# Optimization experiments

Hardware: AMD Instinct MI355X
Metric: run time of the kernel (lower is better)

## Reference

```python
import jax, jax.numpy as jnp
import numpy as np

N = 50000
E = 800000
NODE_IN, EDGE_IN, HID, OUT, L = 32, 16, 128, 128, 2


def _layer_norm(h, g, b, eps=1e-5):
    mu = jnp.mean(h, axis=-1, keepdims=True)
    var = jnp.var(h, axis=-1, keepdims=True)
    return (h - mu) * jax.lax.rsqrt(var + eps) * g + b


def setup_inputs() -> dict:
    key = jax.random.key(0)
    ks = jax.random.split(key, 20)
    s = lambda k, shape, fan: jax.random.normal(k, shape, jnp.float32) * (1.0 / np.sqrt(fan))
    return {
        "x": jax.random.normal(ks[0], (N, NODE_IN), jnp.float32),
        "edge_index": jax.random.randint(ks[1], (2, E), 0, N, jnp.int64),
        "edge_attr": jax.random.normal(ks[2], (E, EDGE_IN), jnp.float32),
        "enc_W": s(ks[3], (NODE_IN, HID), NODE_IN),
        "enc_b": jnp.zeros((HID,), jnp.float32),
        "enc_g": jnp.ones((HID,), jnp.float32),
        "enc_beta": jnp.zeros((HID,), jnp.float32),
        "msg_W1": s(ks[4], (L, 2 * HID + EDGE_IN, HID), 2 * HID + EDGE_IN),
        "msg_b1": jnp.zeros((L, HID), jnp.float32),
        "msg_W2": s(ks[5], (L, HID, HID), HID),
        "msg_b2": jnp.zeros((L, HID), jnp.float32),
        "upd_W1": s(ks[6], (L, 2 * HID, HID), 2 * HID),
        "upd_b1": jnp.zeros((L, HID), jnp.float32),
        "upd_W2": s(ks[7], (L, HID, HID), HID),
        "upd_b2": jnp.zeros((L, HID), jnp.float32),
        "ln_g": jnp.ones((L, HID), jnp.float32),
        "ln_beta": jnp.zeros((L, HID), jnp.float32),
        "head_W": s(ks[8], (HID, OUT), HID),
        "head_b": jnp.zeros((OUT,), jnp.float32),
    }


def reference(x, edge_index, edge_attr, enc_W, enc_b, enc_g, enc_beta,
              msg_W1, msg_b1, msg_W2, msg_b2, upd_W1, upd_b1, upd_W2, upd_b2,
              ln_g, ln_beta, head_W, head_b):
    src = edge_index[0]  # x_j (source)
    tgt = edge_index[1]  # x_i (target, aggregation index)
    n = x.shape[0]

    # node encoder: Linear -> ReLU -> LayerNorm
    h = jax.nn.relu(x @ enc_W + enc_b)
    h = _layer_norm(h, enc_g, enc_beta)

    # per-edge incoming-degree for mean aggregation (isolated nodes -> 0)
    cnt = jax.ops.segment_sum(jnp.ones((tgt.shape[0],), h.dtype), tgt, num_segments=n)
    denom = jnp.maximum(cnt, 1.0)[:, None]

    for l in range(L):
        x_i = h[tgt]                                 # [E, HID]
        x_j = h[src]                                 # [E, HID]
        msg_in = jnp.concatenate([x_i, x_j, edge_attr], axis=-1)  # [E, 2H+Ed]
        m = jax.nn.relu(msg_in @ msg_W1[l] + msg_b1[l]) @ msg_W2[l] + msg_b2[l]
        aggr = jax.ops.segment_sum(m, tgt, num_segments=n) / denom  # mean
        upd_in = jnp.concatenate([h, aggr], axis=-1)
        out = jax.nn.relu(upd_in @ upd_W1[l] + upd_b1[l]) @ upd_W2[l] + upd_b2[l]
        h = _layer_norm(h + out, ln_g[l], ln_beta[l])

    return h @ head_W + head_b
```

## Files before the change

### kernel.cpp

```cpp
#include <hip/hip_runtime.h>
#include <hip/hip_bf16.h>
#include <stdint.h>

#define N_NODES 50000
#define N_EDGES 800000
#define NL 2

#define KS2 136
#define KSU 264
#define ESTR 132

typedef __bf16 bf16x8 __attribute__((ext_vector_type(8)));
typedef float f32x4 __attribute__((ext_vector_type(4)));

__device__ __forceinline__ f32x4 mfma_bf16(uint4 a, uint4 b, f32x4 c) {
    return __builtin_amdgcn_mfma_f32_16x16x32_bf16(
        __builtin_bit_cast(bf16x8, a), __builtin_bit_cast(bf16x8, b), c, 0, 0, 0);
}

__device__ __forceinline__ unsigned short f2b(float f) {
    union { float f; unsigned u; } v; v.f = f;
    unsigned r = v.u + 0x7FFFu + ((v.u >> 16) & 1u);
    return (unsigned short)(r >> 16);
}

__device__ __forceinline__ float b2f(unsigned short u) {
    union { unsigned u; float f; } v; v.u = ((unsigned)u) << 16; return v.f;
}
__device__ __forceinline__ float b2f_lo(unsigned u) {
    union { unsigned u; float f; } v; v.u = u << 16; return v.f;
}
__device__ __forceinline__ float b2f_hi(unsigned u) {
    union { unsigned u; float f; } v; v.u = u & 0xFFFF0000u; return v.f;
}

template<int KSTEPS, int BSTR>
__device__ __forceinline__ void gemm8(const unsigned short* aLane,
                                      const unsigned short* bLane, f32x4 acc[8]) {
#pragma unroll
    for (int kc = 0; kc < KSTEPS; kc++) {
        uint4 a = *(const uint4*)(aLane + kc * 32);
#pragma unroll
        for (int ct = 0; ct < 8; ct++) {
            uint4 b = *(const uint4*)(bLane + (size_t)ct * 16 * BSTR + kc * 32);
            acc[ct] = mfma_bf16(a, b, acc[ct]);
        }
    }
}

template<int KSTEPS, int ASTR, int BSTR>
__device__ __forceinline__ void gemm_2x4(const unsigned short* aLane,
                                         const unsigned short* bLane,
                                         f32x4 acc[4][2]) {
#pragma unroll
    for (int kc = 0; kc < KSTEPS; kc++) {
        uint4 b0 = *(const uint4*)(bLane + kc * 32);
        uint4 b1 = *(const uint4*)(bLane + (size_t)16 * BSTR + kc * 32);
#pragma unroll
        for (int rt = 0; rt < 4; rt++) {
            uint4 a = *(const uint4*)(aLane + (size_t)rt * 16 * ASTR + kc * 32);
            acc[rt][0] = mfma_bf16(a, b0, acc[rt][0]);
            acc[rt][1] = mfma_bf16(a, b1, acc[rt][1]);
        }
    }
}

__global__ void prep_kernel(const float* __restrict__ mW1,
                            const float* __restrict__ uW1, const float* __restrict__ uW2,
                            const float* __restrict__ hW,
                            unsigned short* __restrict__ wab, unsigned short* __restrict__ w1cp,
                            unsigned short* __restrict__ u1t, unsigned short* __restrict__ u2t,
                            unsigned short* __restrict__ ht) {
    int i = blockIdx.x * 256 + threadIdx.x;
    const int SA = NL * 256 * 136;
    const int SC = NL * 128 * 32;
    const int SU = NL * 128 * KSU;
    const int S3 = NL * 128 * KS2;
    const int S4 = 128 * KS2;
    if (i < SA) {
        int l = i / (256 * 136), r = i % (256 * 136), j = r / 136, k = r % 136;
        float v = 0.f;
        if (k < 128)
            v = (j < 128) ? mW1[((size_t)l * 272 + k) * 128 + j]
                          : mW1[((size_t)l * 272 + 128 + k) * 128 + (j - 128)];
        wab[i] = f2b(v);
        return;
    }
    i -= SA;
    if (i < SC) {
        int l = i / (128 * 32), r = i % (128 * 32), j = r / 32, k = r % 32;
        w1cp[i] = (k < 16) ? f2b(mW1[((size_t)l * 272 + 256 + k) * 128 + j]) : (unsigned short)0;
        return;
    }
    i -= SC;
    if (i < SU) {
        int l = i / (128 * KSU), r = i % (128 * KSU), n = r / KSU, k = r % KSU;
        if (k < 128)       u1t[i] = f2b(uW1[((size_t)l * 256 + k) * 128 + n]);
        else if (k >= 256) u1t[i] = 0;
        return;
    }
    i -= SU;
    if (i < S3) {
        int l = i / (128 * KS2), r = i % (128 * KS2), n = r / KS2, k = r % KS2;
        u2t[i] = (k < 128) ? f2b(uW2[((size_t)l * 128 + k) * 128 + n]) : (unsigned short)0;
        return;
    }
    i -= S3;
    if (i < S4) {
        int n = i / KS2, k = i % KS2;
        ht[i] = (k < 128) ? f2b(hW[(size_t)k * 128 + n]) : (unsigned short)0;
    }
}

__global__ void prep2_kernel(const float* __restrict__ mW2, const float* __restrict__ uW1,
                             unsigned short* __restrict__ u1t) {
    __shared__ float w2row[128];
    const int l = blockIdx.x >> 7, j = blockIdx.x & 127;
    const int n = threadIdx.x;
    w2row[n] = mW2[((size_t)l * 128 + j) * 128 + n];
    __syncthreads();
    float s = 0.f;
#pragma unroll 8
    for (int c = 0; c < 128; c++)
        s += w2row[c] * uW1[((size_t)l * 256 + 128 + c) * 128 + n];
    u1t[(size_t)l * 128 * KSU + (size_t)n * KSU + 128 + j] = f2b(s);
}

__global__ void prep3_kernel(const float* __restrict__ mb2, const float* __restrict__ uW1,
                             float* __restrict__ bfold) {
    const int l = blockIdx.x;
    const int n = threadIdx.x;
    float s = 0.f;
#pragma unroll 8
    for (int c = 0; c < 128; c++)
        s += mb2[l * 128 + c] * uW1[((size_t)l * 256 + 128 + c) * 128 + n];
    bfold[l * 128 + n] = s;
}

__global__ __launch_bounds__(256) void enc_kernel(
        const float* __restrict__ x, const float* __restrict__ W,
        const float* __restrict__ b, const float* __restrict__ g, const float* __restrict__ bet,
        float* __restrict__ h, unsigned short* __restrict__ hb) {
    __shared__ float sx[64];
    __shared__ float redS[4], redSS[4];
    const int t = threadIdx.x;
    const int nb = blockIdx.x * 2;
    if (t < 64) sx[t] = x[(size_t)nb * 32 + t];
    __syncthreads();
    const int half = t >> 7, j = t & 127;
    const int node = nb + half;
    float acc = b[j];
#pragma unroll
    for (int k = 0; k < 32; k++) acc += sx[half * 32 + k] * W[k * 128 + j];
    float v = fmaxf(acc, 0.f);
    float s = v, ss = v * v;
#pragma unroll
    for (int d = 32; d > 0; d >>= 1) { s += __shfl_down(s, d); ss += __shfl_down(ss, d); }
    const int wv = t >> 6;
    if ((t & 63) == 0) { redS[wv] = s; redSS[wv] = ss; }
    __syncthreads();
    float S = redS[half * 2] + redS[half * 2 + 1];
    float SS = redSS[half * 2] + redSS[half * 2 + 1];
    float mu = S * (1.f / 128.f);
    float var = SS * (1.f / 128.f) - mu * mu;
    float rs = rsqrtf(var + 1e-5f);
    float o = (v - mu) * rs * g[j] + bet[j];
    h[(size_t)node * 128 + j] = o;
    hb[(size_t)node * 128 + j] = f2b(o);
}

__global__ void hist_kernel(const int* __restrict__ tgt, int* __restrict__ hist) {
    int i = blockIdx.x * 256 + threadIdx.x;
    atomicAdd(hist + tgt[i], 1);
}

__global__ void scan1_kernel(const int* __restrict__ hist, int* __restrict__ incl,
                             int* __restrict__ blksum) {
    __shared__ int buf[256];
    const int t = threadIdx.x;
    const int i = blockIdx.x * 256 + t;
    int v = (i < N_NODES) ? hist[i] : 0;
    buf[t] = v; __syncthreads();
#pragma unroll
    for (int d = 1; d < 256; d <<= 1) {
        int x = (t >= d) ? buf[t - d] : 0;
        __syncthreads();
        buf[t] += x;
        __syncthreads();
    }
    if (i < N_NODES) incl[i] = buf[t];
    if (t == 255) blksum[blockIdx.x] = buf[255];
}

__global__ void scan2_kernel(int* __restrict__ blksum, int nblk) {
    __shared__ int buf[256];
    const int t = threadIdx.x;
    int v = (t < nblk) ? blksum[t] : 0;
    buf[t] = v; __syncthreads();
#pragma unroll
    for (int d = 1; d < 256; d <<= 1) {
        int x = (t >= d) ? buf[t - d] : 0;
        __syncthreads();
        buf[t] += x;
        __syncthreads();
    }
    if (t < nblk) blksum[t] = buf[t];
}

__global__ void scan3_kernel(int* __restrict__ incl, const int* __restrict__ blksum,
                             const int* __restrict__ hist) {
    const int i = blockIdx.x * 256 + threadIdx.x;
    if (i >= N_NODES) return;
    const int b = blockIdx.x;
    const int base = (b > 0) ? blksum[b - 1] : 0;
    incl[i] = incl[i] + base - hist[i];
}

__global__ void scatterp_kernel(const int* __restrict__ src, const int* __restrict__ tgt,
                                int* __restrict__ cursor, uint2* __restrict__ permst) {
    const int e = blockIdx.x * 256 + threadIdx.x;
    const int tg = tgt[e];
    const int p = atomicAdd(cursor + tg, 1);
    permst[p] = make_uint2((unsigned)e, ((unsigned)src[e] << 16) | (unsigned)tg);
}

__global__ __launch_bounds__(256) void gather_kernel(
        const uint2* __restrict__ permst, const float* __restrict__ ea,
        unsigned int* __restrict__ sST, unsigned short* __restrict__ eabS) {
    const int p = blockIdx.x * 256 + threadIdx.x;
    const uint2 v = permst[p];
    sST[p] = v.y;
    const float4* s = (const float4*)(ea + (size_t)v.x * 16);
    ushort4* d = (ushort4*)(eabS + (size_t)p * 16);
#pragma unroll
    for (int i = 0; i < 4; i++) {
        float4 f = s[i];
        d[i] = make_ushort4(f2b(f.x), f2b(f.y), f2b(f.z), f2b(f.w));
    }
}

__global__ __launch_bounds__(256, 4) void node_kernel(
        const unsigned short* __restrict__ hb, const unsigned short* __restrict__ wab,
        const float* __restrict__ b1,
        unsigned short* __restrict__ Tb, unsigned short* __restrict__ Sb) {
    __shared__ __align__(16) unsigned short As[64 * KS2];
    const int t = threadIdx.x;
    const int n0 = blockIdx.x * 64;
    {
        const int m = t >> 2, q = t & 3;
        const int node = n0 + m;
        uint4* dst = (uint4*)(As + m * KS2);
        if (node < N_NODES) {
            const uint4* s = (const uint4*)(hb + (size_t)node * 128);
#pragma unroll
            for (int i = 0; i < 4; i++) dst[q * 4 + i] = s[q * 4 + i];
        } else {
            uint4 z{0, 0, 0, 0};
            for (int i = q; i < 16; i += 4) dst[i] = z;
        }
    }
    __syncthreads();

    const int wv = t >> 6, lane = t & 63, lr = lane & 15, lq = lane >> 4;
    const int cb = wv * 64;
    const f32x4 z4 = {0.f, 0.f, 0.f, 0.f};
    f32x4 acc[4][4];
#pragma unroll
    for (int i = 0; i < 4; i++)
#pragma unroll
        for (int j = 0; j < 4; j++) acc[i][j] = z4;

    const unsigned short* aL = As + lr * KS2 + lq * 8;
    const unsigned short* bL = wab + (size_t)(cb + lr) * KS2 + lq * 8;
#pragma unroll
    for (int kc = 0; kc < 4; kc++) {
        uint4 bA = *(const uint4*)(bL + kc * 32);
        uint4 bB = *(const uint4*)(bL + (size_t)16 * KS2 + kc * 32);
        uint4 bC = *(const uint4*)(bL + (size_t)32 * KS2 + kc * 32);
        uint4 bD = *(const uint4*)(bL + (size_t)48 * KS2 + kc * 32);
#pragma unroll
        for (int rt = 0; rt < 4; rt++) {
            uint4 a = *(const uint4*)(aL + (size_t)rt * 16 * KS2 + kc * 32);
            acc[rt][0] = mfma_bf16(a, bA, acc[rt][0]);
            acc[rt][1] = mfma_bf16(a, bB, acc[rt][1]);
            acc[rt][2] = mfma_bf16(a, bC, acc[rt][2]);
            acc[rt][3] = mfma_bf16(a, bD, acc[rt][3]);
        }
    }
#pragma unroll
    for (int ct = 0; ct < 4; ct++) {
        const int j = cb + ct * 16 + lr;
        const float bias = (j < 128) ? b1[j] : 0.f;
#pragma unroll
        for (int rt = 0; rt < 4; rt++) {
#pragma unroll
            for (int r = 0; r < 4; r++) {
                const int node = n0 + rt * 16 + lq * 4 + r;
                if (node < N_NODES) {
                    const float v = acc[rt][ct][r] + bias;
                    if (j < 128) Tb[(size_t)node * 128 + j] = f2b(v);
                    else         Sb[(size_t)node * 128 + (j - 128)] = f2b(v);
                }
            }
        }
    }
}

__global__ __launch_bounds__(256, 8) void edge_kernel(
        const unsigned short* __restrict__ eabS,
        const unsigned int* __restrict__ sST,
        const unsigned short* __restrict__ w1cp,
        const unsigned short* __restrict__ Tb, const unsigned short* __restrict__ Sb,
        float* __restrict__ aggr) {
    __shared__ __align__(16) float Es[32 * ESTR];
    __shared__ int sT[64];
    __shared__ int sS[64];

    const int t = threadIdx.x;
    const int e0 = blockIdx.x * 64;
    if (t < 64) {
        const unsigned v = sST[e0 + t];
        sT[t] = (int)(v & 0xFFFFu);
        sS[t] = (int)(v >> 16);
    }
    __syncthreads();

    const int wv = t >> 6, lane = t & 63, lr = lane & 15, lq = lane >> 4;
    const int rtw = (wv >> 1) * 16;
    const int cbw = (wv & 1) * 64;
    const int m = t & 31, c8b = t >> 5;
    const f32x4 z4 = {0.f, 0.f, 0.f, 0.f};

    unsigned long long bmask;
    {
        const int l = t & 63;
        const int a = sT[l];
        const int b = (l > 0) ? sT[l - 1] : a;
        bmask = __ballot(a != b);
    }

    uint4 t0a, t0b, s0a, s0b;
    {
        const unsigned short* Tr = Tb + (size_t)sT[m] * 128;
        const unsigned short* Sr = Sb + (size_t)sS[m] * 128;
        t0a = *(const uint4*)(Tr + c8b * 8);
        t0b = *(const uint4*)(Tr + c8b * 8 + 64);
        s0a = *(const uint4*)(Sr + c8b * 8);
        s0b = *(const uint4*)(Sr + c8b * 8 + 64);
    }

    float s = 0.f;
    bool first = true;

    {
        uint4 a = {0, 0, 0, 0};
        if (lq < 2)
            a = *(const uint4*)(eabS + (size_t)(e0 + rtw + lr) * 16 + lq * 8);
        f32x4 acc[4];
#pragma unroll
        for (int ct = 0; ct < 4; ct++) {
            uint4 b = *(const uint4*)(w1cp + (cbw + ct * 16 + lr) * 32 + lq * 8);
            acc[ct] = mfma_bf16(a, b, z4);
        }
#pragma unroll
        for (int ct = 0; ct < 4; ct++) {
            const int col = cbw + ct * 16 + lr;
#pragma unroll
            for (int r = 0; r < 4; r++)
                Es[(rtw + lq * 4 + r) * ESTR + col] = acc[ct][r];
        }
    }
    __syncthreads();

    uint4 t1a, t1b, s1a, s1b;
    {
        float* Erow = Es + m * ESTR;
        float4* EA = (float4*)(Erow + c8b * 8);
        float4* EB = (float4*)(Erow + c8b * 8 + 64);
        float4 ea0 = EA[0], ea1 = EA[1];
        ea0.x = fmaxf(ea0.x + b2f_lo(t0a.x) + b2f_lo(s0a.x), 0.f);
        ea0.y = fmaxf(ea0.y + b2f_hi(t0a.x) + b2f_hi(s0a.x), 0.f);
        ea0.z = fmaxf(ea0.z + b2f_lo(t0a.y) + b2f_lo(s0a.y), 0.f);
        ea0.w = fmaxf(ea0.w + b2f_hi(t0a.y) + b2f_hi(s0a.y), 0.f);
        ea1.x = fmaxf(ea1.x + b2f_lo(t0a.z) + b2f_lo(s0a.z), 0.f);
        ea1.y = fmaxf(ea1.y + b2f_hi(t0a.z) + b2f_hi(s0a.z), 0.f);
        ea1.z = fmaxf(ea1.z + b2f_lo(t0a.w) + b2f_lo(s0a.w), 0.f);
        ea1.w = fmaxf(ea1.w + b2f_hi(t0a.w) + b2f_hi(s0a.w), 0.f);
        EA[0] = ea0; EA[1] = ea1;
        float4 eb0 = EB[0], eb1 = EB[1];
        eb0.x = fmaxf(eb0.x + b2f_lo(t0b.x) + b2f_lo(s0b.x), 0.f);
        eb0.y = fmaxf(eb0.y + b2f_hi(t0b.x) + b2f_hi(s0b.x), 0.f);
        eb0.z = fmaxf(eb0.z + b2f_lo(t0b.y) + b2f_lo(s0b.y), 0.f);
        eb0.w = fmaxf(eb0.w + b2f_hi(t0b.y) + b2f_hi(s0b.y), 0.f);
        eb1.x = fmaxf(eb1.x + b2f_lo(t0b.z) + b2f_lo(s0b.z), 0.f);
        eb1.y = fmaxf(eb1.y + b2f_hi(t0b.z) + b2f_hi(s0b.z), 0.f);
        eb1.z = fmaxf(eb1.z + b2f_lo(t0b.w) + b2f_lo(s0b.w), 0.f);
        eb1.w = fmaxf(eb1.w + b2f_hi(t0b.w) + b2f_hi(s0b.w), 0.f);
        EB[0] = eb0; EB[1] = eb1;

        const unsigned short* Tr = Tb + (size_t)sT[32 + m] * 128;
        const unsigned short* Sr = Sb + (size_t)sS[32 + m] * 128;
        t1a = *(const uint4*)(Tr + c8b * 8);
        t1b = *(const uint4*)(Tr + c8b * 8 + 64);
        s1a = *(const uint4*)(Sr + c8b * 8);
        s1b = *(const uint4*)(Sr + c8b * 8 + 64);
    }
    __syncthreads();

    if (t < 128) {
        const int c = t;
        const unsigned mh = (unsigned)bmask;
#pragma unroll
        for (int i8 = 0; i8 < 4; i8++) {
            float v[8];
#pragma unroll
            for (int j = 0; j < 8; j++) v[j] = Es[(i8 * 8 + j) * ESTR + c];
#pragma unroll
            for (int j = 0; j < 8; j++) {
                const int i = i8 * 8 + j;
                if (mh & (1u << i)) {
                    float* dst = aggr + (size_t)sT[i - 1] * 128 + c;
                    if (first) { atomicAdd(dst, s); first = false; }
                    else       { *dst = s; }
                    s = 0.f;
                }
                s += v[j];
            }
        }
    }
    __syncthreads();

    {
        uint4 a = {0, 0, 0, 0};
        if (lq < 2)
            a = *(const uint4*)(eabS + (size_t)(e0 + 32 + rtw + lr) * 16 + lq * 8);
        f32x4 acc[4];
#pragma unroll
        for (int ct = 0; ct < 4; ct++) {
            uint4 b = *(const uint4*)(w1cp + (cbw + ct * 16 + lr) * 32 + lq * 8);
            acc[ct] = mfma_bf16(a, b, z4);
        }
#pragma unroll
        for (int ct = 0; ct < 4; ct++) {
            const int col = cbw + ct * 16 + lr;
#pragma unroll
            for (int r = 0; r < 4; r++)
                Es[(rtw + lq * 4 + r) * ESTR + col] = acc[ct][r];
        }
    }
    __syncthreads();

    {
        float* Erow = Es + m * ESTR;
        float4* EA = (float4*)(Erow + c8b * 8);
        float4* EB = (float4*)(Erow + c8b * 8 + 64);
        float4 ea0 = EA[0], ea1 = EA[1];
        ea0.x = fmaxf(ea0.x + b2f_lo(t1a.x) + b2f_lo(s1a.x), 0.f);
        ea0.y = fmaxf(ea0.y + b2f_hi(t1a.x) + b2f_hi(s1a.x), 0.f);
        ea0.z = fmaxf(ea0.z + b2f_lo(t1a.y) + b2f_lo(s1a.y), 0.f);
        ea0.w = fmaxf(ea0.w + b2f_hi(t1a.y) + b2f_hi(s1a.y), 0.f);
        ea1.x = fmaxf(ea1.x + b2f_lo(t1a.z) + b2f_lo(s1a.z), 0.f);
        ea1.y = fmaxf(ea1.y + b2f_hi(t1a.z) + b2f_hi(s1a.z), 0.f);
        ea1.z = fmaxf(ea1.z + b2f_lo(t1a.w) + b2f_lo(s1a.w), 0.f);
        ea1.w = fmaxf(ea1.w + b2f_hi(t1a.w) + b2f_hi(s1a.w), 0.f);
        EA[0] = ea0; EA[1] = ea1;
        float4 eb0 = EB[0], eb1 = EB[1];
        eb0.x = fmaxf(eb0.x + b2f_lo(t1b.x) + b2f_lo(s1b.x), 0.f);
        eb0.y = fmaxf(eb0.y + b2f_hi(t1b.x) + b2f_hi(s1b.x), 0.f);
        eb0.z = fmaxf(eb0.z + b2f_lo(t1b.y) + b2f_lo(s1b.y), 0.f);
        eb0.w = fmaxf(eb0.w + b2f_hi(t1b.y) + b2f_hi(s1b.y), 0.f);
        eb1.x = fmaxf(eb1.x + b2f_lo(t1b.z) + b2f_lo(s1b.z), 0.f);
        eb1.y = fmaxf(eb1.y + b2f_hi(t1b.z) + b2f_hi(s1b.z), 0.f);
        eb1.z = fmaxf(eb1.z + b2f_lo(t1b.w) + b2f_lo(s1b.w), 0.f);
        eb1.w = fmaxf(eb1.w + b2f_hi(t1b.w) + b2f_hi(s1b.w), 0.f);
        EB[0] = eb0; EB[1] = eb1;
    }
    __syncthreads();

    if (t < 128) {
        const int c = t;
        const unsigned mh = (unsigned)(bmask >> 32);
#pragma unroll
        for (int i8 = 0; i8 < 4; i8++) {
            float v[8];
#pragma unroll
            for (int j = 0; j < 8; j++) v[j] = Es[(i8 * 8 + j) * ESTR + c];
#pragma unroll
            for (int j = 0; j < 8; j++) {
                const int i = i8 * 8 + j;
                if (mh & (1u << i)) {
                    float* dst = aggr + (size_t)sT[32 + i - 1] * 128 + c;
                    if (first) { atomicAdd(dst, s); first = false; }
                    else       { *dst = s; }
                    s = 0.f;
                }
                s += v[j];
            }
        }
        atomicAdd(aggr + (size_t)sT[63] * 128 + c, s);
    }
}

__global__ __launch_bounds__(256, 4) void upd_kernel(
        const unsigned short* __restrict__ hb_in, const float* __restrict__ h_in,
        const float* __restrict__ aggr, const int* __restrict__ hist,
        const unsigned short* __restrict__ u1t, const unsigned short* __restrict__ u2t,
        const float* __restrict__ b1, const float* __restrict__ bf,
        const float* __restrict__ b2,
        const float* __restrict__ g, const float* __restrict__ bet,
        float* __restrict__ h_out, unsigned short* __restrict__ hb_out) {
    __shared__ __align__(16) char smemA[64 * KSU * 2];
    __shared__ float sF[64];
    unsigned short* As = (unsigned short*)smemA;
    float* LNb = (float*)smemA;

    const int t = threadIdx.x;
    const int n0 = blockIdx.x * 64;
    {
        const int m = t >> 2, q = t & 3;
        const int node = n0 + m;
        unsigned short* row = As + m * KSU;
        if (node < N_NODES) {
            const uint4* ph = (const uint4*)(hb_in + (size_t)node * 128);
            uint4* d0 = (uint4*)row;
#pragma unroll
            for (int i = 0; i < 4; i++) d0[q * 4 + i] = ph[q * 4 + i];
            const int cntv = hist[node];
            if (q == 0) sF[m] = (cntv > 0) ? 1.f : 0.f;
            const float rden = 1.0f / fmaxf((float)cntv, 1.0f);
            const float4* pa = (const float4*)(aggr + (size_t)node * 128 + q * 32);
            ushort4* d1 = (ushort4*)(row + 128 + q * 32);
#pragma unroll
            for (int i = 0; i < 8; i++) {
                float4 v = pa[i];
                d1[i] = make_ushort4(f2b(v.x * rden), f2b(v.y * rden),
                                     f2b(v.z * rden), f2b(v.w * rden));
            }
            if (q == 0) { uint4 z{0, 0, 0, 0}; ((uint4*)(row + 256))[0] = z; }
        } else {
            if (q == 0) sF[m] = 0.f;
            uint4 z{0, 0, 0, 0};
            uint4* d = (uint4*)row;
            for (int i = q; i < 33; i += 4) d[i] = z;
        }
    }
    __syncthreads();

    const int wv = t >> 6, lane = t & 63, lr = lane & 15, lq = lane >> 4;
    const int cb = wv * 32;
    const f32x4 z4 = {0.f, 0.f, 0.f, 0.f};

    f32x4 acc[4][2];
#pragma unroll
    for (int i = 0; i < 4; i++) { acc[i][0] = z4; acc[i][1] = z4; }
    gemm_2x4<8, KSU, KSU>(As + lr * KSU + lq * 8,
                          u1t + (size_t)(cb + lr) * KSU + lq * 8, acc);
    __syncthreads();

#pragma unroll
    for (int ct = 0; ct < 2; ct++) {
        const int col = cb + ct * 16 + lr;
        const float bv = b1[col];
        const float bfv = bf[col];
#pragma unroll
        for (int rt = 0; rt < 4; rt++) {
#pragma unroll
            for (int r = 0; r < 4; r++) {
                const int ml = rt * 16 + lq * 4 + r;
                float v = fmaxf(acc[rt][ct][r] + bv + sF[ml] * bfv, 0.f);
                As[ml * KSU + col] = f2b(v);
            }
        }
    }
    __syncthreads();

    f32x4 acc2[4][2];
#pragma unroll
    for (int i = 0; i < 4; i++) { acc2[i][0] = z4; acc2[i][1] = z4; }
    gemm_2x4<4, KSU, KS2>(As + lr * KSU + lq * 8,
                          u2t + (size_t)(cb + lr) * KS2 + lq * 8, acc2);
    __syncthreads();

#pragma unroll
    for (int ct = 0; ct < 2; ct++) {
        const int col = cb + ct * 16 + lr;
        const float bv = b2[col];
#pragma unroll
        for (int rt = 0; rt < 4; rt++) {
#pragma unroll
            for (int r = 0; r < 4; r++) {
                const int ml = rt * 16 + lq * 4 + r;
                const int node = n0 + ml;
                if (node < N_NODES)
                    LNb[ml * 132 + col] = acc2[rt][ct][r] + bv + h_in[(size_t)node * 128 + col];
            }
        }
    }
    __syncthreads();

    {
        const int r = t >> 2, c0 = (t & 3) * 32;
        const int node = n0 + r;
        if (node < N_NODES) {
            float s = 0.f, ss = 0.f;
#pragma unroll
            for (int i = 0; i < 32; i++) { float v = LNb[r * 132 + c0 + i]; s += v; ss += v * v; }
            s += __shfl_xor(s, 1); ss += __shfl_xor(ss, 1);
            s += __shfl_xor(s, 2); ss += __shfl_xor(ss, 2);
            const float mu = s * (1.0f / 128.0f);
            const float var = ss * (1.0f / 128.0f) - mu * mu;
            const float rs = rsqrtf(var + 1e-5f);
#pragma unroll
            for (int i = 0; i < 32; i++) {
                const int j = c0 + i;
                float v = (LNb[r * 132 + j] - mu) * rs * g[j] + bet[j];
                h_out[(size_t)node * 128 + j] = v;
                hb_out[(size_t)node * 128 + j] = f2b(v);
            }
        }
    }
}

__global__ __launch_bounds__(256, 2) void head_kernel(
        const unsigned short* __restrict__ hb, const unsigned short* __restrict__ ht,
        const float* __restrict__ hbias, float* __restrict__ out) {
    __shared__ __align__(16) unsigned short As[64 * KS2];
    const int t = threadIdx.x;
    const int n0 = blockIdx.x * 64;
    {
        const int m = t >> 2, q = t & 3;
        const int node = n0 + m;
        uint4* dst = (uint4*)(As + m * KS2);
        if (node < N_NODES) {
            const uint4* s = (const uint4*)(hb + (size_t)node * 128);
#pragma unroll
            for (int i = 0; i < 4; i++) dst[q * 4 + i] = s[q * 4 + i];
        } else {
            uint4 z{0, 0, 0, 0};
            for (int i = q; i < 16; i += 4) dst[i] = z;
        }
    }
    __syncthreads();

    const int wv = t >> 6, lane = t & 63, lr = lane & 15, lq = lane >> 4;
    const int m0 = wv * 16;
    const f32x4 z4 = {0.f, 0.f, 0.f, 0.f};
    f32x4 acc[8];
#pragma unroll
    for (int i = 0; i < 8; i++) acc[i] = z4;
    gemm8<4, KS2>(As + (m0 + lr) * KS2 + lq * 8, ht + (size_t)lr * KS2 + lq * 8, acc);
#pragma unroll
    for (int ct = 0; ct < 8; ct++) {
        const int col = ct * 16 + lr;
        const float bv = hbias[col];
#pragma unroll
        for (int r = 0; r < 4; r++) {
            const int node = n0 + m0 + lq * 4 + r;
            if (node < N_NODES) out[(size_t)node * 128 + col] = acc[ct][r] + bv;
        }
    }
}

extern "C" void kernel_launch(void* const* d_in, const int* in_sizes, int n_in,
                              void* d_out, int out_size, void* d_ws, size_t ws_size,
                              hipStream_t stream) {
    const float* x       = (const float*)d_in[0];
    const int*   ei      = (const int*)d_in[1];
    const float* ea      = (const float*)d_in[2];
    const float* encW    = (const float*)d_in[3];
    const float* encb    = (const float*)d_in[4];
    const float* encg    = (const float*)d_in[5];
    const float* encbeta = (const float*)d_in[6];
    const float* msgW1   = (const float*)d_in[7];
    const float* msgb1   = (const float*)d_in[8];
    const float* msgW2   = (const float*)d_in[9];
    const float* msgb2   = (const float*)d_in[10];
    const float* updW1   = (const float*)d_in[11];
    const float* updb1   = (const float*)d_in[12];
    const float* updW2   = (const float*)d_in[13];
    const float* updb2   = (const float*)d_in[14];
    const float* lng     = (const float*)d_in[15];
    const float* lnbeta  = (const float*)d_in[16];
    const float* headW   = (const float*)d_in[17];
    const float* headb   = (const float*)d_in[18];

    char* w = (char*)d_ws;
    size_t off = 0;
    auto nxt = [&](size_t bytes) -> void* {
        void* p = w + off;
        off = (off + bytes + 255) & ~(size_t)255;
        return p;
    };
    float*          h     = (float*)nxt((size_t)N_NODES * 128 * 4);
    unsigned short* hb    = (unsigned short*)nxt((size_t)N_NODES * 128 * 2);
    float*          aggr  = (float*)nxt((size_t)N_NODES * 128 * 4);
    unsigned short* Tb    = (unsigned short*)nxt((size_t)N_NODES * 128 * 2);
    unsigned short* Sb    = (unsigned short*)nxt((size_t)N_NODES * 128 * 2);
    unsigned short* eabS  = (unsigned short*)nxt((size_t)N_EDGES * 16 * 2);
    unsigned int*   sST   = (unsigned int*)nxt((size_t)N_EDGES * 4);
    int*            hist  = (int*)nxt((size_t)N_NODES * 4);
    int*            incl  = (int*)nxt((size_t)N_NODES * 4);
    int*            blksum= (int*)nxt(256 * 4);
    unsigned short* wab   = (unsigned short*)nxt((size_t)NL * 256 * 136 * 2);
    unsigned short* w1cp  = (unsigned short*)nxt((size_t)NL * 128 * 32 * 2);
    unsigned short* u1t   = (unsigned short*)nxt((size_t)NL * 128 * KSU * 2);
    unsigned short* u2t   = (unsigned short*)nxt((size_t)NL * 128 * KS2 * 2);
    unsigned short* ht    = (unsigned short*)nxt((size_t)128 * KS2 * 2);
    float*          bfold = (float*)nxt((size_t)NL * 128 * 4);

    uint2*          permst = (uint2*)aggr;

    const int NBLK = (N_NODES + 255) / 256;
    const int PREP_N = NL * 256 * 136 + NL * 128 * 32 + NL * 128 * KSU
                     + NL * 128 * KS2 + 128 * KS2;

    hipMemsetAsync(hist, 0, (size_t)N_NODES * 4, stream);
    prep_kernel<<<(PREP_N + 255) / 256, 256, 0, stream>>>(msgW1, updW1, updW2, headW,
                                                          wab, w1cp, u1t, u2t, ht);
    prep2_kernel<<<NL * 128, 128, 0, stream>>>(msgW2, updW1, u1t);
    prep3_kernel<<<NL, 128, 0, stream>>>(msgb2, updW1, bfold);
    enc_kernel<<<25000, 256, 0, stream>>>(x, encW, encb, encg, encbeta, h, hb);
    hist_kernel<<<3125, 256, 0, stream>>>(ei + N_EDGES, hist);
    scan1_kernel<<<NBLK, 256, 0, stream>>>(hist, incl, blksum);
    scan2_kernel<<<1, 256, 0, stream>>>(blksum, NBLK);
    scan3_kernel<<<NBLK, 256, 0, stream>>>(incl, blksum, hist);
    scatterp_kernel<<<3125, 256, 0, stream>>>(ei, ei + N_EDGES, incl, permst);
    gather_kernel<<<3125, 256, 0, stream>>>(permst, ea, sST, eabS);

    for (int l = 0; l < NL; l++) {
        node_kernel<<<782, 256, 0, stream>>>(hb, wab + (size_t)l * 256 * 136,
                                             msgb1 + l * 128, Tb, Sb);
        hipMemsetAsync(aggr, 0, (size_t)N_NODES * 128 * 4, stream);
        edge_kernel<<<12500, 256, 0, stream>>>(eabS, sST,
                                               w1cp + (size_t)l * 128 * 32,
                                               Tb, Sb, aggr);
        upd_kernel<<<782, 256, 0, stream>>>(hb, h, aggr, hist,
                                            u1t + (size_t)l * 128 * KSU,
                                            u2t + (size_t)l * 128 * KS2,
                                            updb1 + l * 128, bfold + l * 128,
                                            updb2 + l * 128,
                                            lng + l * 128, lnbeta + l * 128, h, hb);
    }
    head_kernel<<<782, 256, 0, stream>>>(hb, ht, headb, (float*)d_out);
}
```

Baseline: 550.5 us.

## Swizzle edge LDS tile and fuse head GEMM into final update kernel

In the edge kernel, the fp32 staging tile gets an XOR swizzle keyed on row, and gathered rows are remapped to 8 threads per edge, to cut LDS bank conflicts on both the MFMA-result stores and the row-wise vector reads. In the last layer, the update kernel now runs the output-head GEMM itself, reusing its shared memory for the bf16 normalized rows. This removes the separate head kernel launch and the final h/hb writes. The fused path adds two syncs and a 32-float register buffer per thread, which may raise register pressure in the update kernel.

```diff
diff --git a/kernel.cpp b/kernel.cpp
--- a/kernel.cpp
+++ b/kernel.cpp
@@ -328,7 +328,9 @@
     const int wv = t >> 6, lane = t & 63, lr = lane & 15, lq = lane >> 4;
     const int rtw = (wv >> 1) * 16;
     const int cbw = (wv & 1) * 64;
-    const int m = t & 31, c8b = t >> 5;
+    const int m = t >> 3;
+    const int q = t & 7;
+    const int sw = (m & 7) << 3;
     const f32x4 z4 = {0.f, 0.f, 0.f, 0.f};
 
     unsigned long long bmask;
@@ -343,10 +345,10 @@
     {
         const unsigned short* Tr = Tb + (size_t)sT[m] * 128;
         const unsigned short* Sr = Sb + (size_t)sS[m] * 128;
-        t0a = *(const uint4*)(Tr + c8b * 8);
-        t0b = *(const uint4*)(Tr + c8b * 8 + 64);
-        s0a = *(const uint4*)(Sr + c8b * 8);
-        s0b = *(const uint4*)(Sr + c8b * 8 + 64);
+        t0a = *(const uint4*)(Tr + q * 8);
+        t0b = *(const uint4*)(Tr + 64 + q * 8);
+        s0a = *(const uint4*)(Sr + q * 8);
+        s0b = *(const uint4*)(Sr + 64 + q * 8);
     }
 
     float s = 0.f;
@@ -366,8 +368,10 @@
         for (int ct = 0; ct < 4; ct++) {
             const int col = cbw + ct * 16 + lr;
 #pragma unroll
-            for (int r = 0; r < 4; r++)
-                Es[(rtw + lq * 4 + r) * ESTR + col] = acc[ct][r];
+            for (int r = 0; r < 4; r++) {
+                const int row = rtw + lq * 4 + r;
+                Es[row * ESTR + (col ^ ((row & 7) << 3))] = acc[ct][r];
+            }
         }
     }
     __syncthreads();
@@ -375,8 +379,8 @@
     uint4 t1a, t1b, s1a, s1b;
     {
         float* Erow = Es + m * ESTR;
-        float4* EA = (float4*)(Erow + c8b * 8);
-        float4* EB = (float4*)(Erow + c8b * 8 + 64);
+        float4* EA = (float4*)(Erow + ((q * 8) ^ sw));
+        float4* EB = (float4*)(Erow + 64 + ((q * 8) ^ sw));
         float4 ea0 = EA[0], ea1 = EA[1];
         ea0.x = fmaxf(ea0.x + b2f_lo(t0a.x) + b2f_lo(s0a.x), 0.f);
         ea0.y = fmaxf(ea0.y + b2f_hi(t0a.x) + b2f_hi(s0a.x), 0.f);
@@ -400,10 +404,10 @@
 
         const unsigned short* Tr = Tb + (size_t)sT[32 + m] * 128;
         const unsigned short* Sr = Sb + (size_t)sS[32 + m] * 128;
-        t1a = *(const uint4*)(Tr + c8b * 8);
-        t1b = *(const uint4*)(Tr + c8b * 8 + 64);
-        s1a = *(const uint4*)(Sr + c8b * 8);
-        s1b = *(const uint4*)(Sr + c8b * 8 + 64);
+        t1a = *(const uint4*)(Tr + q * 8);
+        t1b = *(const uint4*)(Tr + 64 + q * 8);
+        s1a = *(const uint4*)(Sr + q * 8);
+        s1b = *(const uint4*)(Sr + 64 + q * 8);
     }
     __syncthreads();
 
@@ -414,7 +418,10 @@
         for (int i8 = 0; i8 < 4; i8++) {
             float v[8];
 #pragma unroll
-            for (int j = 0; j < 8; j++) v[j] = Es[(i8 * 8 + j) * ESTR + c];
+            for (int j = 0; j < 8; j++) {
+                const int i = i8 * 8 + j;
+                v[j] = Es[i * ESTR + (c ^ ((i & 7) << 3))];
+            }
 #pragma unroll
             for (int j = 0; j < 8; j++) {
                 const int i = i8 * 8 + j;
@@ -444,16 +451,18 @@
         for (int ct = 0; ct < 4; ct++) {
             const int col = cbw + ct * 16 + lr;
 #pragma unroll
-            for (int r = 0; r < 4; r++)
-                Es[(rtw + lq * 4 + r) * ESTR + col] = acc[ct][r];
+            for (int r = 0; r < 4; r++) {
+                const int row = rtw + lq * 4 + r;
+                Es[row * ESTR + (col ^ ((row & 7) << 3))] = acc[ct][r];
+            }
         }
     }
     __syncthreads();
 
     {
         float* Erow = Es + m * ESTR;
-        float4* EA = (float4*)(Erow + c8b * 8);
-        float4* EB = (float4*)(Erow + c8b * 8 + 64);
+        float4* EA = (float4*)(Erow + ((q * 8) ^ sw));
+        float4* EB = (float4*)(Erow + 64 + ((q * 8) ^ sw));
         float4 ea0 = EA[0], ea1 = EA[1];
         ea0.x = fmaxf(ea0.x + b2f_lo(t1a.x) + b2f_lo(s1a.x), 0.f);
         ea0.y = fmaxf(ea0.y + b2f_hi(t1a.x) + b2f_hi(s1a.x), 0.f);
@@ -484,7 +493,10 @@
         for (int i8 = 0; i8 < 4; i8++) {
             float v[8];
 #pragma unroll
-            for (int j = 0; j < 8; j++) v[j] = Es[(i8 * 8 + j) * ESTR + c];
+            for (int j = 0; j < 8; j++) {
+                const int i = i8 * 8 + j;
+                v[j] = Es[i * ESTR + (c ^ ((i & 7) << 3))];
+            }
 #pragma unroll
             for (int j = 0; j < 8; j++) {
                 const int i = i8 * 8 + j;
@@ -508,7 +520,9 @@
         const float* __restrict__ b1, const float* __restrict__ bf,
         const float* __restrict__ b2,
         const float* __restrict__ g, const float* __restrict__ bet,
-        float* __restrict__ h_out, unsigned short* __restrict__ hb_out) {
+        float* __restrict__ h_out, unsigned short* __restrict__ hb_out,
+        const unsigned short* __restrict__ ht, const float* __restrict__ hbias,
+        float* __restrict__ out, const int fuse) {
     __shared__ __align__(16) char smemA[64 * KSU * 2];
     __shared__ float sF[64];
     unsigned short* As = (unsigned short*)smemA;
@@ -601,7 +615,9 @@
     {
         const int r = t >> 2, c0 = (t & 3) * 32;
         const int node = n0 + r;
-        if (node < N_NODES) {
+        const bool valid = (node < N_NODES);
+        float vbuf[32];
+        if (valid) {
             float s = 0.f, ss = 0.f;
 #pragma unroll
             for (int i = 0; i < 32; i++) { float v = LNb[r * 132 + c0 + i]; s += v; ss += v * v; }
@@ -613,50 +629,40 @@
 #pragma unroll
             for (int i = 0; i < 32; i++) {
                 const int j = c0 + i;
-                float v = (LNb[r * 132 + j] - mu) * rs * g[j] + bet[j];
-                h_out[(size_t)node * 128 + j] = v;
-                hb_out[(size_t)node * 128 + j] = f2b(v);
-            }
-        }
-    }
-}
-
-__global__ __launch_bounds__(256, 2) void head_kernel(
-        const unsigned short* __restrict__ hb, const unsigned short* __restrict__ ht,
-        const float* __restrict__ hbias, float* __restrict__ out) {
-    __shared__ __align__(16) unsigned short As[64 * KS2];
-    const int t = threadIdx.x;
-    const int n0 = blockIdx.x * 64;
-    {
-        const int m = t >> 2, q = t & 3;
-        const int node = n0 + m;
-        uint4* dst = (uint4*)(As + m * KS2);
-        if (node < N_NODES) {
-            const uint4* s = (const uint4*)(hb + (size_t)node * 128);
-#pragma unroll
-            for (int i = 0; i < 4; i++) dst[q * 4 + i] = s[q * 4 + i];
-        } else {
-            uint4 z{0, 0, 0, 0};
-            for (int i = q; i < 16; i += 4) dst[i] = z;
-        }
-    }
-    __syncthreads();
-
-    const int wv = t >> 6, lane = t & 63, lr = lane & 15, lq = lane >> 4;
-    const int m0 = wv * 16;
-    const f32x4 z4 = {0.f, 0.f, 0.f, 0.f};
-    f32x4 acc[8];
-#pragma unroll
-    for (int i = 0; i < 8; i++) acc[i] = z4;
-    gemm8<4, KS2>(As + (m0 + lr) * KS2 + lq * 8, ht + (size_t)lr * KS2 + lq * 8, acc);
-#pragma unroll
-    for (int ct = 0; ct < 8; ct++) {
-        const int col = ct * 16 + lr;
-        const float bv = hbias[col];
-#pragma unroll
-        for (int r = 0; r < 4; r++) {
-            const int node = n0 + m0 + lq * 4 + r;
-            if (node < N_NODES) out[(size_t)node * 128 + col] = acc[ct][r] + bv;
+                vbuf[i] = (LNb[r * 132 + j] - mu) * rs * g[j] + bet[j];
+            }
+            if (!fuse) {
+#pragma unroll
+                for (int i = 0; i < 32; i++) {
+                    const int j = c0 + i;
+                    h_out[(size_t)node * 128 + j] = vbuf[i];
+                    hb_out[(size_t)node * 128 + j] = f2b(vbuf[i]);
+                }
+            }
+        }
+        if (fuse) {
+            __syncthreads();
+            unsigned short* Ah = (unsigned short*)smemA;
+#pragma unroll
+            for (int i = 0; i < 32; i++)
+                Ah[r * KS2 + c0 + i] = valid ? f2b(vbuf[i]) : (unsigned short)0;
+            __syncthreads();
+            const int m0 = wv * 16;
+            f32x4 hacc[8];
+#pragma unroll
+            for (int i = 0; i < 8; i++) hacc[i] = z4;
+            gemm8<4, KS2>(Ah + (size_t)(m0 + lr) * KS2 + lq * 8,
+                          ht + (size_t)lr * KS2 + lq * 8, hacc);
+#pragma unroll
+            for (int ct = 0; ct < 8; ct++) {
+                const int col = ct * 16 + lr;
+                const float bv = hbias[col];
+#pragma unroll
+                for (int r2 = 0; r2 < 4; r2++) {
+                    const int node2 = n0 + m0 + lq * 4 + r2;
+                    if (node2 < N_NODES) out[(size_t)node2 * 128 + col] = hacc[ct][r2] + bv;
+                }
+            }
         }
     }
 }
@@ -739,7 +745,8 @@
                                             u2t + (size_t)l * 128 * KS2,
                                             updb1 + l * 128, bfold + l * 128,
                                             updb2 + l * 128,
-                                            lng + l * 128, lnbeta + l * 128, h, hb);
-    }
-    head_kernel<<<782, 256, 0, stream>>>(hb, ht, headb, (float*)d_out);
-}
+                                            lng + l * 128, lnbeta + l * 128, h, hb,
+                                            ht, headb, (float*)d_out,
+                                            (l == NL - 1) ? 1 : 0);
+    }
+}
```

Result: no change. 554.0 us (+0.6%).
